# Kernel tuning notes

Hardware: AMD Instinct MI355X
Metric: run time of the kernel (lower is better)

Reference implementation:

```python
import jax, jax.numpy as jnp
import numpy as np

N, M, D = 8192, 65536, 512

def setup_inputs() -> dict:
    key = jax.random.key(0)
    k1, k2 = jax.random.split(key)
    embedding = jax.random.normal(k1, (N, D), dtype=jnp.float32)
    memory_bank = jax.random.normal(k2, (M, D), dtype=jnp.float32)
    return {"embedding": embedding, "memory_bank": memory_bank}

def reference(embedding, memory_bank):
    # torch.cdist(embedding, memory_bank, p=2.0) via the expansion
    x_sq = jnp.sum(embedding * embedding, axis=1, keepdims=True)        # [N, 1]
    m_sq = jnp.sum(memory_bank * memory_bank, axis=1)[None, :]          # [1, M]
    cross = embedding @ memory_bank.T                                    # [N, M]
    dist_sq = jnp.maximum(x_sq + m_sq - 2.0 * cross, 0.0)
    distances = jnp.sqrt(dist_sq)                                        # [N, M]
    # distances.topk(k=1, largest=False, dim=1) -> per-row min, kept dim
    patch_scores = jnp.min(distances, axis=1, keepdims=True)             # [N, 1]
    return patch_scores
```

## Files before the change

### kernel.cpp

```cpp
#include <hip/hip_runtime.h>
#include <stdint.h>

#define NROWS 8192
#define MROWS 65536
#define DDIM  512

#define BM 256
#define BN 256
#define BKK 32
#define CT 8
#define KT_PER_CT (DDIM / BKK)
#define NT (CT * KT_PER_CT)
#define GRID_X ((NROWS / BM) * (MROWS / (BN * CT)))

typedef __attribute__((ext_vector_type(4))) float f32x4;
typedef __attribute__((ext_vector_type(8))) short short8;
typedef unsigned short ushort_t;
typedef unsigned int   uint_t;

__device__ __forceinline__ ushort_t f2bf(float x) {
    uint_t u = __float_as_uint(x);
    u += 0x7fffu + ((u >> 16) & 1u);
    return (ushort_t)(u >> 16);
}
__device__ __forceinline__ float bf2f(ushort_t b) {
    return __uint_as_float(((uint_t)b) << 16);
}

__device__ __forceinline__ void gll16(const void* g, void* l) {
    __builtin_amdgcn_global_load_lds((__attribute__((address_space(1))) void*)g,
                                     (__attribute__((address_space(3))) void*)l,
                                     16, 0, 0);
}

#define SBAR()  __builtin_amdgcn_s_barrier()
#define SCHED0() __builtin_amdgcn_sched_barrier(0)

__global__ void init_minsq(uint_t* minsq) {
    int i = blockIdx.x * 256 + threadIdx.x;
    if (i < NROWS) minsq[i] = 0x7f800000u;
}

__global__ void convert_norms(const float* __restrict__ emb, const float* __restrict__ mem,
                              ushort_t* __restrict__ Abf, ushort_t* __restrict__ Bbf,
                              float* __restrict__ xsq, float* __restrict__ msq) {
    unsigned gid = blockIdx.x * 256 + threadIdx.x;
    unsigned row = gid >> 6;
    unsigned within = gid & 63u;
    unsigned seg = within >> 2, cc = within & 3u;
    int lane = threadIdx.x & 63;
    const float* src; ushort_t* dst; float* nrm; unsigned r;
    if (row < NROWS) { r = row;         src = emb + (size_t)r * DDIM; dst = Abf + (size_t)r * DDIM; nrm = xsq + r; }
    else             { r = row - NROWS; src = mem + (size_t)r * DDIM; dst = Bbf + (size_t)r * DDIM; nrm = msq + r; }
    unsigned scc = cc ^ ((r >> 1) & 3u);
    const float4* s4 = (const float4*)(src + seg * 32 + scc * 8);
    float4 a = s4[0], b = s4[1];
    ushort_t q[8];
    q[0]=f2bf(a.x); q[1]=f2bf(a.y); q[2]=f2bf(a.z); q[3]=f2bf(a.w);
    q[4]=f2bf(b.x); q[5]=f2bf(b.y); q[6]=f2bf(b.z); q[7]=f2bf(b.w);
    uint4 w;
    w.x = (uint_t)q[0] | ((uint_t)q[1] << 16);
    w.y = (uint_t)q[2] | ((uint_t)q[3] << 16);
    w.z = (uint_t)q[4] | ((uint_t)q[5] << 16);
    w.w = (uint_t)q[6] | ((uint_t)q[7] << 16);
    *(uint4*)(dst + seg * 32 + cc * 8) = w;
    float s = 0.f;
    #pragma unroll
    for (int i = 0; i < 8; ++i) { float v = bf2f(q[i]); s += v * v; }
    #pragma unroll
    for (int o = 1; o < 64; o <<= 1) s += __shfl_xor(s, o);
    if (lane == 0) *nrm = s;
}

__global__ __launch_bounds__(512, 2) void gemm256_min(
    const ushort_t* __restrict__ Abf, const ushort_t* __restrict__ Bbf,
    const float* __restrict__ xsq, const float* __restrict__ msq,
    uint_t* __restrict__ minsq)
{
    __shared__ alignas(16) ushort_t As[2][BM * BKK];
    __shared__ alignas(16) ushort_t Bs[2][BN * BKK];

    const int tid  = threadIdx.x;
    const int lane = tid & 63;
    const int wave = tid >> 6;
    const int wm   = wave >> 2;
    const int wn   = wave & 3;
    const int laneRow = lane & 15;
    const int laneK   = lane >> 4;

    unsigned wg  = blockIdx.x;
    unsigned swz = (wg & 7u) * (GRID_X / 8) + (wg >> 3);
    const unsigned rt = swz & 31u;
    const unsigned cg = swz >> 5;
    const size_t r0    = (size_t)rt * BM;
    const size_t cbase = (size_t)cg * (BN * CT);

    const int chunk = ((laneK ^ ((laneRow >> 1) & 3)) << 4);
    int offA[8], offB[4];
    #pragma unroll
    for (int m = 0; m < 8; ++m) offA[m] = (wm * 128 + m * 16 + laneRow) * 64 + chunk;
    #pragma unroll
    for (int n = 0; n < 4; ++n) offB[n] = (wn * 64 + n * 16 + laneRow) * 64 + chunk;

    const int rowoff = wave * 16 + (lane >> 2);
    const int inrow  = (lane & 3) * 16;
    const char* Ag = (const char*)Abf + (r0 + rowoff) * 1024 + inrow;

    f32x4 acc[8][4];
    float runmin[8][4];
    #pragma unroll
    for (int m = 0; m < 8; ++m)
        #pragma unroll
        for (int n = 0; n < 4; ++n) { acc[m][n] = (f32x4)0.f; runmin[m][n] = 3.0e38f; }

    {
        const char* Asrc = Ag;
        const char* Bsrc = (const char*)Bbf + (cbase + rowoff) * 1024 + inrow;
        char* Ad = (char*)&As[0][0] + wave * 1024;
        char* Bd = (char*)&Bs[0][0] + wave * 1024;
        gll16(Asrc, Ad);                     gll16(Bsrc, Bd);
        gll16(Asrc + 131072, Ad + 8192);     gll16(Bsrc + 131072, Bd + 8192);
        asm volatile("s_waitcnt vmcnt(0)" ::: "memory");
        SCHED0(); SBAR(); SCHED0();
    }

    for (int t = 0; t < NT; ++t) {
        const int cur = t & 1;
        const char* AbC = (const char*)&As[cur][0];
        const char* BbC = (const char*)&Bs[cur][0];
        const bool stg = (t + 1) < NT;
        const char* AsrcN = nullptr; const char* BsrcN = nullptr;
        char* AdN = nullptr; char* BdN = nullptr;
        if (stg) {
            int t2 = t + 1;
            int ks2 = t2 & 15, ct2 = t2 >> 4;
            AsrcN = Ag + (size_t)ks2 * 64;
            BsrcN = (const char*)Bbf + (cbase + (size_t)ct2 * BN + rowoff) * 1024 + inrow + (size_t)ks2 * 64;
            AdN = (char*)&As[cur ^ 1][0] + wave * 1024;
            BdN = (char*)&Bs[cur ^ 1][0] + wave * 1024;
        }

        short8 af[4], bfr[4];
        #pragma unroll
        for (int m = 0; m < 4; ++m) af[m]  = *(const short8*)(AbC + offA[m]);
        #pragma unroll
        for (int n = 0; n < 4; ++n) bfr[n] = *(const short8*)(BbC + offB[n]);
        if (stg) { gll16(AsrcN, AdN); gll16(BsrcN, BdN); }
        SCHED0(); SBAR(); SCHED0();
        asm volatile("s_waitcnt lgkmcnt(0)" ::: "memory");
        SCHED0();
        __builtin_amdgcn_s_setprio(1);
        #pragma unroll
        for (int m = 0; m < 4; ++m)
            #pragma unroll
            for (int n = 0; n < 4; ++n)
                acc[m][n] = __builtin_amdgcn_mfma_f32_16x16x32_bf16(af[m], bfr[n], acc[m][n], 0, 0, 0);
        __builtin_amdgcn_s_setprio(0);
        SCHED0(); SBAR(); SCHED0();

        short8 ag[4];
        #pragma unroll
        for (int m = 0; m < 4; ++m) ag[m] = *(const short8*)(AbC + offA[m + 4]);
        if (stg) { gll16(AsrcN + 131072, AdN + 8192); gll16(BsrcN + 131072, BdN + 8192); }
        SCHED0(); SBAR(); SCHED0();
        asm volatile("s_waitcnt lgkmcnt(0)" ::: "memory");
        SCHED0();
        __builtin_amdgcn_s_setprio(1);
        #pragma unroll
        for (int m = 0; m < 4; ++m)
            #pragma unroll
            for (int n = 0; n < 4; ++n)
                acc[m + 4][n] = __builtin_amdgcn_mfma_f32_16x16x32_bf16(ag[m], bfr[n], acc[m + 4][n], 0, 0, 0);
        __builtin_amdgcn_s_setprio(0);
        SCHED0();
        asm volatile("s_waitcnt vmcnt(0)" ::: "memory");
        SCHED0(); SBAR(); SCHED0();

        if ((t & 15) == 15) {
            const size_t c0 = cbase + (size_t)(t >> 4) * BN;
            float mc[4];
            #pragma unroll
            for (int n = 0; n < 4; ++n) mc[n] = msq[c0 + wn * 64 + n * 16 + laneRow];
            #pragma unroll
            for (int m = 0; m < 8; ++m)
                #pragma unroll
                for (int n = 0; n < 4; ++n) {
                    #pragma unroll
                    for (int j = 0; j < 4; ++j)
                        runmin[m][j] = fminf(runmin[m][j], fmaf(-2.f, acc[m][n][j], mc[n]));
                    acc[m][n] = (f32x4)0.f;
                }
        }
    }

    #pragma unroll
    for (int m = 0; m < 8; ++m)
        #pragma unroll
        for (int j = 0; j < 4; ++j) {
            float v = runmin[m][j];
            v = fminf(v, __shfl_xor(v, 1));
            v = fminf(v, __shfl_xor(v, 2));
            v = fminf(v, __shfl_xor(v, 4));
            v = fminf(v, __shfl_xor(v, 8));
            if ((lane & 15) == 0) {
                int grow = (int)r0 + wm * 128 + m * 16 + laneK * 4 + j;
                float d2 = fmaxf(v + xsq[grow], 0.f);
                atomicMin(&minsq[grow], __float_as_uint(d2));
            }
        }
}

__global__ void finish_kernel(const uint_t* __restrict__ minsq, float* __restrict__ out) {
    int i = blockIdx.x * 256 + threadIdx.x;
    if (i < NROWS) out[i] = sqrtf(__uint_as_float(minsq[i]));
}

__global__ void norms_kernel(const float* __restrict__ emb, const float* __restrict__ mem,
                             float* __restrict__ xsq, float* __restrict__ msq) {
    int row  = blockIdx.x * 4 + (threadIdx.x >> 6);
    int lane = threadIdx.x & 63;
    const float* src; float* dst;
    if (row < NROWS) { src = emb + (size_t)row * DDIM;           dst = xsq + row; }
    else             { src = mem + (size_t)(row - NROWS) * DDIM; dst = msq + (row - NROWS); }
    float4 f0 = *(const float4*)(src + lane * 8);
    float4 f1 = *(const float4*)(src + lane * 8 + 4);
    float s = 0.f, v;
    v = bf2f(f2bf(f0.x)); s += v*v;  v = bf2f(f2bf(f0.y)); s += v*v;
    v = bf2f(f2bf(f0.z)); s += v*v;  v = bf2f(f2bf(f0.w)); s += v*v;
    v = bf2f(f2bf(f1.x)); s += v*v;  v = bf2f(f2bf(f1.y)); s += v*v;
    v = bf2f(f2bf(f1.z)); s += v*v;  v = bf2f(f2bf(f1.w)); s += v*v;
    #pragma unroll
    for (int o = 1; o < 64; o <<= 1) s += __shfl_xor(s, o);
    if (lane == 0) *dst = s;
}

__device__ __forceinline__ void fb_stage_load(const float* __restrict__ emb,
                                              const float* __restrict__ mem,
                                              size_t r0, size_t c0, int ks,
                                              float4* ra, float4* rb, int tid) {
    #pragma unroll
    for (int p = 0; p < 4; ++p) {
        int row = p * 32 + (tid >> 3);
        int c   = (tid & 7) * 8;
        const float* sa = emb + (r0 + row) * DDIM + ks * 64 + c;
        const float* sb = mem + (c0 + row) * DDIM + ks * 64 + c;
        ra[2*p]   = *(const float4*)sa;  ra[2*p+1] = *(const float4*)(sa + 4);
        rb[2*p]   = *(const float4*)sb;  rb[2*p+1] = *(const float4*)(sb + 4);
    }
}
__device__ __forceinline__ void fb_stage_write(ushort_t* Ab, ushort_t* Bb,
                                               const float4* ra, const float4* rb, int tid) {
    #pragma unroll
    for (int p = 0; p < 4; ++p) {
        int row = p * 32 + (tid >> 3);
        int ccs = (tid & 7) ^ (row & 7);
        uint4 wa, wb;
        wa.x = (uint_t)f2bf(ra[2*p].x)   | ((uint_t)f2bf(ra[2*p].y)   << 16);
        wa.y = (uint_t)f2bf(ra[2*p].z)   | ((uint_t)f2bf(ra[2*p].w)   << 16);
        wa.z = (uint_t)f2bf(ra[2*p+1].x) | ((uint_t)f2bf(ra[2*p+1].y) << 16);
        wa.w = (uint_t)f2bf(ra[2*p+1].z) | ((uint_t)f2bf(ra[2*p+1].w) << 16);
        wb.x = (uint_t)f2bf(rb[2*p].x)   | ((uint_t)f2bf(rb[2*p].y)   << 16);
        wb.y = (uint_t)f2bf(rb[2*p].z)   | ((uint_t)f2bf(rb[2*p].w)   << 16);
        wb.z = (uint_t)f2bf(rb[2*p+1].x) | ((uint_t)f2bf(rb[2*p+1].y) << 16);
        wb.w = (uint_t)f2bf(rb[2*p+1].z) | ((uint_t)f2bf(rb[2*p+1].w) << 16);
        *(uint4*)&Ab[row * 64 + ccs * 8] = wa;
        *(uint4*)&Bb[row * 64 + ccs * 8] = wb;
    }
}

__global__ __launch_bounds__(256, 2) void gemm_min_fb(
    const float* __restrict__ emb, const float* __restrict__ mem,
    const float* __restrict__ xsq, const float* __restrict__ msq,
    uint_t* __restrict__ minsq)
{
    __shared__ alignas(16) ushort_t Ab[128 * 64];
    __shared__ alignas(16) ushort_t Bb[128 * 64];
    const int tid = threadIdx.x, lane = tid & 63, wave = tid >> 6;
    const int wm = wave >> 1, wn = wave & 1;
    unsigned wg = blockIdx.x;
    unsigned swz = (wg & 7u) * (2048 / 8) + (wg >> 3);
    const unsigned rt = swz & 63u, cgf = swz >> 6;
    const size_t r0 = (size_t)rt * 128;
    float runmin[4][4];
    #pragma unroll
    for (int m = 0; m < 4; ++m)
        #pragma unroll
        for (int j = 0; j < 4; ++j) runmin[m][j] = 3.0e38f;
    float4 ra[8], rb[8];
    for (int ctf = 0; ctf < 16; ++ctf) {
        const size_t c0 = ((size_t)cgf * 16 + ctf) * 128;
        f32x4 acc[4][4] = {};
        fb_stage_load(emb, mem, r0, c0, 0, ra, rb, tid);
        for (int ks = 0; ks < 8; ++ks) {
            __syncthreads();
            fb_stage_write(Ab, Bb, ra, rb, tid);
            if (ks + 1 < 8) fb_stage_load(emb, mem, r0, c0, ks + 1, ra, rb, tid);
            __syncthreads();
            #pragma unroll
            for (int kk = 0; kk < 2; ++kk) {
                short8 af[4], bfm[4];
                #pragma unroll
                for (int m = 0; m < 4; ++m) {
                    int r = wm * 64 + m * 16 + (lane & 15);
                    int c = ((kk * 4 + (lane >> 4)) ^ (r & 7)) * 8;
                    af[m] = *(const short8*)&Ab[r * 64 + c];
                }
                #pragma unroll
                for (int n = 0; n < 4; ++n) {
                    int r = wn * 64 + n * 16 + (lane & 15);
                    int c = ((kk * 4 + (lane >> 4)) ^ (r & 7)) * 8;
                    bfm[n] = *(const short8*)&Bb[r * 64 + c];
                }
                #pragma unroll
                for (int m = 0; m < 4; ++m)
                    #pragma unroll
                    for (int n = 0; n < 4; ++n)
                        acc[m][n] = __builtin_amdgcn_mfma_f32_16x16x32_bf16(af[m], bfm[n], acc[m][n], 0, 0, 0);
            }
        }
        float mc[4];
        #pragma unroll
        for (int n = 0; n < 4; ++n) mc[n] = msq[c0 + wn * 64 + n * 16 + (lane & 15)];
        #pragma unroll
        for (int m = 0; m < 4; ++m)
            #pragma unroll
            for (int n = 0; n < 4; ++n)
                #pragma unroll
                for (int j = 0; j < 4; ++j)
                    runmin[m][j] = fminf(runmin[m][j], fmaf(-2.f, acc[m][n][j], mc[n]));
    }
    #pragma unroll
    for (int m = 0; m < 4; ++m)
        #pragma unroll
        for (int j = 0; j < 4; ++j) {
            float v = runmin[m][j];
            v = fminf(v, __shfl_xor(v, 1));
            v = fminf(v, __shfl_xor(v, 2));
            v = fminf(v, __shfl_xor(v, 4));
            v = fminf(v, __shfl_xor(v, 8));
            if ((lane & 15) == 0) {
                int grow = (int)r0 + wm * 64 + m * 16 + (lane >> 4) * 4 + j;
                float d2 = fmaxf(v + xsq[grow], 0.f);
                atomicMin(&minsq[grow], __float_as_uint(d2));
            }
        }
}

extern "C" void kernel_launch(void* const* d_in, const int* in_sizes, int n_in,
                              void* d_out, int out_size, void* d_ws, size_t ws_size,
                              hipStream_t stream) {
    const float* emb = (const float*)d_in[0];
    const float* mem = (const float*)d_in[1];
    float* out = (float*)d_out;

    char* ws = (char*)d_ws;
    float*  xsq   = (float*)ws;
    float*  msq   = (float*)(ws + 32768);
    uint_t* minsq = (uint_t*)(ws + 32768 + 262144);
    ushort_t* Abf = (ushort_t*)(ws + 327680);
    ushort_t* Bbf = Abf + (size_t)NROWS * DDIM;
    const size_t NEED = 327680 + ((size_t)NROWS + MROWS) * DDIM * 2;

    init_minsq<<<(NROWS + 255) / 256, 256, 0, stream>>>(minsq);
    if (ws_size >= NEED) {
        convert_norms<<<((NROWS + MROWS) * 64) / 256, 256, 0, stream>>>(emb, mem, Abf, Bbf, xsq, msq);
        gemm256_min<<<GRID_X, 512, 0, stream>>>(Abf, Bbf, xsq, msq, minsq);
    } else {
        norms_kernel<<<(NROWS + MROWS) / 4, 256, 0, stream>>>(emb, mem, xsq, msq);
        gemm_min_fb<<<2048, 256, 0, stream>>>(emb, mem, xsq, msq, minsq);
    }
    finish_kernel<<<(NROWS + 255) / 256, 256, 0, stream>>>(minsq, out);
}
```

Before: 593.7 us.

## Double K-step per iteration with split LDS buffers and fewer barriers

Each main-loop iteration now handles two 32-wide K slices held in two LDS sub-buffers, doubling shared memory per stage. Global-to-LDS loads for the next stage are interleaved with MFMA phases, and partial vmcnt waits replace full drains. This cuts barriers per K element from four per 32-K step to two per 64-K step. The msq loads for the fold are hoisted earlier to hide their latency. The larger LDS footprint (128KB per block) may lower occupancy below the two blocks per CU the launch bounds request.

```diff
diff --git a/kernel.cpp b/kernel.cpp
--- a/kernel.cpp
+++ b/kernel.cpp
@@ -7,10 +7,9 @@
 
 #define BM 256
 #define BN 256
-#define BKK 32
 #define CT 8
-#define KT_PER_CT (DDIM / BKK)
-#define NT (CT * KT_PER_CT)
+#define KS_PER_CT 8
+#define NT (CT * KS_PER_CT)
 #define GRID_X ((NROWS / BM) * (MROWS / (BN * CT)))
 
 typedef __attribute__((ext_vector_type(4))) float f32x4;
@@ -33,7 +32,7 @@
                                      16, 0, 0);
 }
 
-#define SBAR()  __builtin_amdgcn_s_barrier()
+#define SBAR()   __builtin_amdgcn_s_barrier()
 #define SCHED0() __builtin_amdgcn_sched_barrier(0)
 
 __global__ void init_minsq(uint_t* minsq) {
@@ -77,8 +76,8 @@
     const float* __restrict__ xsq, const float* __restrict__ msq,
     uint_t* __restrict__ minsq)
 {
-    __shared__ alignas(16) ushort_t As[2][BM * BKK];
-    __shared__ alignas(16) ushort_t Bs[2][BN * BKK];
+    __shared__ alignas(16) ushort_t As[2][2][256 * 32];
+    __shared__ alignas(16) ushort_t Bs[2][2][256 * 32];
 
     const int tid  = threadIdx.x;
     const int lane = tid & 63;
@@ -104,7 +103,7 @@
 
     const int rowoff = wave * 16 + (lane >> 2);
     const int inrow  = (lane & 3) * 16;
-    const char* Ag = (const char*)Abf + (r0 + rowoff) * 1024 + inrow;
+    const char* Agb = (const char*)Abf + (r0 + rowoff) * 1024 + inrow;
 
     f32x4 acc[8][4];
     float runmin[8][4];
@@ -114,39 +113,89 @@
         for (int n = 0; n < 4; ++n) { acc[m][n] = (f32x4)0.f; runmin[m][n] = 3.0e38f; }
 
     {
-        const char* Asrc = Ag;
-        const char* Bsrc = (const char*)Bbf + (cbase + rowoff) * 1024 + inrow;
-        char* Ad = (char*)&As[0][0] + wave * 1024;
-        char* Bd = (char*)&Bs[0][0] + wave * 1024;
-        gll16(Asrc, Ad);                     gll16(Bsrc, Bd);
-        gll16(Asrc + 131072, Ad + 8192);     gll16(Bsrc + 131072, Bd + 8192);
-        asm volatile("s_waitcnt vmcnt(0)" ::: "memory");
+        const char* gB = (const char*)Bbf + (cbase + rowoff) * 1024 + inrow;
+        char* lA0 = (char*)&As[0][0][0] + wave * 1024;
+        char* lB0 = (char*)&Bs[0][0][0] + wave * 1024;
+        char* lA1 = (char*)&As[0][1][0] + wave * 1024;
+        char* lB1 = (char*)&Bs[0][1][0] + wave * 1024;
+        gll16(Agb,           lA0); gll16(Agb + 131072,      lA0 + 8192);
+        gll16(gB,            lB0); gll16(gB + 131072,       lB0 + 8192);
+        gll16(Agb + 64,      lA1); gll16(Agb + 64 + 131072, lA1 + 8192);
+        gll16(gB + 64,       lB1); gll16(gB + 64 + 131072,  lB1 + 8192);
+    }
+
+    float mc[4] = {0.f, 0.f, 0.f, 0.f};
+
+    for (int t = 0; t < NT; ++t) {
+        const int cur = t & 1, nxt = cur ^ 1;
+        const bool stg = (t + 1) < NT;
+        const bool foldt = (t & 7) == 7;
+        const int ks1 = (t + 1) & 7;
+        const size_t ct1 = (size_t)((t + 1) >> 3);
+        const char* gA1 = Agb + ks1 * 128;
+        const char* gB1 = (const char*)Bbf + (cbase + ct1 * BN + rowoff) * 1024 + inrow + ks1 * 128;
+
+        const char* A0 = (const char*)&As[cur][0][0];
+        const char* A1 = (const char*)&As[cur][1][0];
+        const char* B0 = (const char*)&Bs[cur][0][0];
+        const char* B1 = (const char*)&Bs[cur][1][0];
+
+        short8 af[4], bf[4];
+
+        asm volatile("s_waitcnt vmcnt(4)" ::: "memory");
         SCHED0(); SBAR(); SCHED0();
-    }
-
-    for (int t = 0; t < NT; ++t) {
-        const int cur = t & 1;
-        const char* AbC = (const char*)&As[cur][0];
-        const char* BbC = (const char*)&Bs[cur][0];
-        const bool stg = (t + 1) < NT;
-        const char* AsrcN = nullptr; const char* BsrcN = nullptr;
-        char* AdN = nullptr; char* BdN = nullptr;
+        #pragma unroll
+        for (int m = 0; m < 4; ++m) af[m] = *(const short8*)(A0 + offA[m]);
+        #pragma unroll
+        for (int n = 0; n < 4; ++n) bf[n] = *(const short8*)(B0 + offB[n]);
         if (stg) {
-            int t2 = t + 1;
-            int ks2 = t2 & 15, ct2 = t2 >> 4;
-            AsrcN = Ag + (size_t)ks2 * 64;
-            BsrcN = (const char*)Bbf + (cbase + (size_t)ct2 * BN + rowoff) * 1024 + inrow + (size_t)ks2 * 64;
-            AdN = (char*)&As[cur ^ 1][0] + wave * 1024;
-            BdN = (char*)&Bs[cur ^ 1][0] + wave * 1024;
-        }
-
-        short8 af[4], bfr[4];
-        #pragma unroll
-        for (int m = 0; m < 4; ++m) af[m]  = *(const short8*)(AbC + offA[m]);
-        #pragma unroll
-        for (int n = 0; n < 4; ++n) bfr[n] = *(const short8*)(BbC + offB[n]);
-        if (stg) { gll16(AsrcN, AdN); gll16(BsrcN, BdN); }
+            char* l = (char*)&As[nxt][0][0] + wave * 1024;
+            gll16(gA1, l); gll16(gA1 + 131072, l + 8192);
+        }
+        asm volatile("s_waitcnt lgkmcnt(0)" ::: "memory");
+        SCHED0();
+        __builtin_amdgcn_s_setprio(1);
+        #pragma unroll
+        for (int m = 0; m < 4; ++m)
+            #pragma unroll
+            for (int n = 0; n < 4; ++n)
+                acc[m][n] = __builtin_amdgcn_mfma_f32_16x16x32_bf16(af[m], bf[n], acc[m][n], 0, 0, 0);
+        __builtin_amdgcn_s_setprio(0);
+        SCHED0();
+
+        #pragma unroll
+        for (int m = 0; m < 4; ++m) af[m] = *(const short8*)(A0 + offA[m + 4]);
+        if (stg) {
+            char* l = (char*)&Bs[nxt][0][0] + wave * 1024;
+            gll16(gB1, l); gll16(gB1 + 131072, l + 8192);
+        }
+        if (foldt) {
+            const size_t c0f = cbase + (size_t)(t >> 3) * BN;
+            #pragma unroll
+            for (int n = 0; n < 4; ++n) mc[n] = msq[c0f + wn * 64 + n * 16 + laneRow];
+        }
+        asm volatile("s_waitcnt lgkmcnt(0)" ::: "memory");
+        SCHED0();
+        __builtin_amdgcn_s_setprio(1);
+        #pragma unroll
+        for (int m = 0; m < 4; ++m)
+            #pragma unroll
+            for (int n = 0; n < 4; ++n)
+                acc[m + 4][n] = __builtin_amdgcn_mfma_f32_16x16x32_bf16(af[m], bf[n], acc[m + 4][n], 0, 0, 0);
+        __builtin_amdgcn_s_setprio(0);
+        SCHED0();
+
+        if (stg) { asm volatile("s_waitcnt vmcnt(4)" ::: "memory"); }
+        else     { asm volatile("s_waitcnt vmcnt(0)" ::: "memory"); }
         SCHED0(); SBAR(); SCHED0();
+        #pragma unroll
+        for (int m = 0; m < 4; ++m) af[m] = *(const short8*)(A1 + offA[m]);
+        #pragma unroll
+        for (int n = 0; n < 4; ++n) bf[n] = *(const short8*)(B1 + offB[n]);
+        if (stg) {
+            char* l = (char*)&As[nxt][1][0] + wave * 1024;
+            gll16(gA1 + 64, l); gll16(gA1 + 64 + 131072, l + 8192);
+        }
         asm volatile("s_waitcnt lgkmcnt(0)" ::: "memory");
         SCHED0();
         __builtin_amdgcn_s_setprio(1);
@@ -154,15 +203,16 @@
         for (int m = 0; m < 4; ++m)
             #pragma unroll
             for (int n = 0; n < 4; ++n)
-                acc[m][n] = __builtin_amdgcn_mfma_f32_16x16x32_bf16(af[m], bfr[n], acc[m][n], 0, 0, 0);
+                acc[m][n] = __builtin_amdgcn_mfma_f32_16x16x32_bf16(af[m], bf[n], acc[m][n], 0, 0, 0);
         __builtin_amdgcn_s_setprio(0);
-        SCHED0(); SBAR(); SCHED0();
-
-        short8 ag[4];
-        #pragma unroll
-        for (int m = 0; m < 4; ++m) ag[m] = *(const short8*)(AbC + offA[m + 4]);
-        if (stg) { gll16(AsrcN + 131072, AdN + 8192); gll16(BsrcN + 131072, BdN + 8192); }
-        SCHED0(); SBAR(); SCHED0();
+        SCHED0();
+
+        #pragma unroll
+        for (int m = 0; m < 4; ++m) af[m] = *(const short8*)(A1 + offA[m + 4]);
+        if (stg) {
+            char* l = (char*)&Bs[nxt][1][0] + wave * 1024;
+            gll16(gB1 + 64, l); gll16(gB1 + 64 + 131072, l + 8192);
+        }
         asm volatile("s_waitcnt lgkmcnt(0)" ::: "memory");
         SCHED0();
         __builtin_amdgcn_s_setprio(1);
@@ -170,17 +220,11 @@
         for (int m = 0; m < 4; ++m)
             #pragma unroll
             for (int n = 0; n < 4; ++n)
-                acc[m + 4][n] = __builtin_amdgcn_mfma_f32_16x16x32_bf16(ag[m], bfr[n], acc[m + 4][n], 0, 0, 0);
+                acc[m + 4][n] = __builtin_amdgcn_mfma_f32_16x16x32_bf16(af[m], bf[n], acc[m + 4][n], 0, 0, 0);
         __builtin_amdgcn_s_setprio(0);
         SCHED0();
-        asm volatile("s_waitcnt vmcnt(0)" ::: "memory");
-        SCHED0(); SBAR(); SCHED0();
-
-        if ((t & 15) == 15) {
-            const size_t c0 = cbase + (size_t)(t >> 4) * BN;
-            float mc[4];
-            #pragma unroll
-            for (int n = 0; n < 4; ++n) mc[n] = msq[c0 + wn * 64 + n * 16 + laneRow];
+
+        if (foldt) {
             #pragma unroll
             for (int m = 0; m < 8; ++m)
                 #pragma unroll
@@ -318,16 +362,16 @@
                         acc[m][n] = __builtin_amdgcn_mfma_f32_16x16x32_bf16(af[m], bfm[n], acc[m][n], 0, 0, 0);
             }
         }
-        float mc[4];
-        #pragma unroll
-        for (int n = 0; n < 4; ++n) mc[n] = msq[c0 + wn * 64 + n * 16 + (lane & 15)];
+        float mcf[4];
+        #pragma unroll
+        for (int n = 0; n < 4; ++n) mcf[n] = msq[c0 + wn * 64 + n * 16 + (lane & 15)];
         #pragma unroll
         for (int m = 0; m < 4; ++m)
             #pragma unroll
             for (int n = 0; n < 4; ++n)
                 #pragma unroll
                 for (int j = 0; j < 4; ++j)
-                    runmin[m][j] = fminf(runmin[m][j], fmaf(-2.f, acc[m][n][j], mc[n]));
+                    runmin[m][j] = fminf(runmin[m][j], fmaf(-2.f, acc[m][n][j], mcf[n]));
     }
     #pragma unroll
     for (int m = 0; m < 4; ++m)
```

New measurement: 636.7 us. 7.2% more time.
